# Kernel optimization log

Measured on AMD Instinct MI355X. Metric: run time of the kernel, lower is better.

Reference implementation:

```python
import jax, jax.numpy as jnp
import numpy as np

B, V, C, H, W, N = 2, 5, 32, 256, 320, 40000


def setup_inputs() -> dict:
    key = jax.random.key(0)
    k1, k2, k3, k4 = jax.random.split(key, 4)
    feature_maps = jax.random.normal(k1, (B, V, C, H, W), dtype=jnp.float32)
    # points with z in [1,4] and normalized image coords mostly inside the frustum
    z = jax.random.uniform(k2, (B, N), minval=1.0, maxval=4.0)
    xn = jax.random.uniform(k3, (B, N), minval=-0.55, maxval=0.55)
    yn = jax.random.uniform(k4, (B, N), minval=-0.45, maxval=0.45)
    pts = jnp.stack([xn * z, yn * z, z], axis=1)  # [B, 3, N]
    f = float(W)
    K = jnp.array([[f, 0.0, W / 2.0], [0.0, f, H / 2.0], [0.0, 0.0, 1.0]], jnp.float32)
    cam_intrinsics = jnp.broadcast_to(K, (B, V, 3, 3)).astype(jnp.float32)
    E = jnp.concatenate([jnp.eye(3, dtype=jnp.float32), jnp.zeros((3, 1), jnp.float32)], axis=1)
    cam_extrinsics = jnp.broadcast_to(E, (B, V, 3, 4)).astype(jnp.float32)
    return {"feature_maps": feature_maps, "pts": pts,
            "cam_intrinsics": cam_intrinsics, "cam_extrinsics": cam_extrinsics}


def _bilinear(fm_flat, gx, gy):
    """grid_sample, mode='bilinear', padding_mode='zeros', align_corners=False.
    fm_flat: [BV, C, H*W]; gx, gy: [BV, N] in [-1, 1]. Returns [BV, C, N]."""
    ix = ((gx + 1.0) * W - 1.0) * 0.5
    iy = ((gy + 1.0) * H - 1.0) * 0.5
    x0 = jnp.floor(ix)
    y0 = jnp.floor(iy)
    wx = ix - x0
    wy = iy - y0
    x0i = x0.astype(jnp.int32)
    y0i = y0.astype(jnp.int32)
    out = jnp.zeros((fm_flat.shape[0], fm_flat.shape[1], gx.shape[1]), fm_flat.dtype)
    corners = ((0, 0, (1.0 - wx) * (1.0 - wy)), (1, 0, wx * (1.0 - wy)),
               (0, 1, (1.0 - wx) * wy), (1, 1, wx * wy))
    for dx, dy, w in corners:
        xc = x0i + dx
        yc = y0i + dy
        valid = (xc >= 0) & (xc < W) & (yc >= 0) & (yc < H)
        idx = jnp.clip(yc, 0, H - 1) * W + jnp.clip(xc, 0, W - 1)  # [BV, N]
        v = jnp.take_along_axis(fm_flat, idx[:, None, :], axis=2)  # [BV, C, N]
        out = out + v * (w * valid)[:, None, :]
    return out


def _forward(feature_maps, pts, cam_intrinsics, cam_extrinsics):
    BV = B * V
    fm = feature_maps.reshape(BV, C, H, W)
    Km = cam_intrinsics.reshape(BV, 3, 3)
    Em = cam_extrinsics.reshape(BV, 3, 4)
    R = Em[:, :, :3]
    t = Em[:, :, 3:]
    pe = jnp.broadcast_to(pts[:, None], (B, V, 3, N)).reshape(BV, 3, N)
    tp = (R @ pe + t).transpose(0, 2, 1)  # [BV, N, 3] camera-space points
    x, y, z = tp[..., 0], tp[..., 1], tp[..., 2]
    nuv = jnp.stack([x / z, y / z, jnp.ones_like(x)], axis=-1)  # [BV, N, 3]
    uv = jnp.einsum('bnj,bij->bni', nuv, Km)[..., :2]  # pixel coords
    gx = (uv[..., 0] - 0.5) / (W - 1) * 2.0 - 1.0
    gy = (uv[..., 1] - 0.5) / (H - 1) * 2.0 - 1.0
    dx = 2.0 / (W - 1)
    dy = 2.0 / (H - 1)
    fm_flat = fm.reshape(BV, C, H * W)
    feat = _bilinear(fm_flat, gx, gy)
    fl = _bilinear(fm_flat, gx - dx, gy)
    fr = _bilinear(fm_flat, gx + dx, gy)
    ft = _bilinear(fm_flat, gx, gy - dy)
    fb = _bilinear(fm_flat, gx, gy + dy)
    grad_x = 0.5 * (fr - fl)
    grad_y = 0.5 * (fb - ft)
    pts_feature = feat.reshape(B, V, C, N)
    pts_feature_grad = jnp.stack([grad_x, grad_y], axis=-1).reshape(B, V, C, N, 2)
    return pts_feature, pts_feature_grad


def reference(feature_maps, pts, cam_intrinsics, cam_extrinsics):
    return _forward(feature_maps, pts, cam_intrinsics, cam_extrinsics)
```

## Files before the change

### kernel.cpp

```cpp
#include <hip/hip_runtime.h>

#define Bc 2
#define Vc 5
#define Cc 32
#define Hc 256
#define Wc 320
#define Nc 40000
#define HWc (Hc * Wc)

typedef float v2f __attribute__((ext_vector_type(2)));

__device__ __forceinline__ unsigned bf16_rn(float x) {
    unsigned u = __float_as_uint(x);
    return (u + 0x7fffu + ((u >> 16) & 1u)) >> 16;
}

__global__ void __launch_bounds__(256)
transpose_bf16_kernel(const float* __restrict__ fm, unsigned short* __restrict__ fmT)
{
    __shared__ float tile[Cc][65];
    const int bv  = blockIdx.y;
    const int hw0 = blockIdx.x * 64;
    const int t   = threadIdx.x;

    const int tx = t & 63;
    const int ty = t >> 6;
    const float* src = fm + (size_t)bv * Cc * HWc + hw0;
    #pragma unroll
    for (int i = 0; i < 8; ++i) {
        int c = ty * 8 + i;
        tile[c][tx] = __builtin_nontemporal_load(&src[(size_t)c * HWc + tx]);
    }
    __syncthreads();

    const int cq = t & 3;
    const int hw = t >> 2;
    unsigned r[4];
    #pragma unroll
    for (int j = 0; j < 4; ++j) {
        float a = tile[cq * 8 + 2 * j][hw];
        float b = tile[cq * 8 + 2 * j + 1][hw];
        r[j] = bf16_rn(a) | (bf16_rn(b) << 16);
    }
    const int half = cq >> 1;
    const int sub  = cq & 1;
    uint4* dst = (uint4*)fmT
               + ((size_t)(bv * 2 + half) * HWc + (hw0 + hw)) * 2 + sub;
    *dst = make_uint4(r[0], r[1], r[2], r[3]);
}

__device__ __forceinline__ void corner_setup(float ix, float iy, float coef,
                                             float wk[4], int pix[4])
{
    float x0f = floorf(ix), y0f = floorf(iy);
    float wx = ix - x0f, wy = iy - y0f;
    int x0 = (int)x0f, y0 = (int)y0f;
    float wg0 = (1.0f - wx) * (1.0f - wy);
    float wg1 = wx * (1.0f - wy);
    float wg2 = (1.0f - wx) * wy;
    float wg3 = wx * wy;
    float wg[4] = {wg0, wg1, wg2, wg3};
    #pragma unroll
    for (int k = 0; k < 4; ++k) {
        int xc = x0 + (k & 1);
        int yc = y0 + (k >> 1);
        bool valid = (xc >= 0) & (xc < Wc) & (yc >= 0) & (yc < Hc);
        wk[k] = valid ? coef * wg[k] : 0.0f;
        int xcl = min(max(xc, 0), Wc - 1);
        int ycl = min(max(yc, 0), Hc - 1);
        pix[k] = ycl * Wc + xcl;
    }
}

#define NBLK 6250
#define XQ   781
#define XR   2

__global__ void __launch_bounds__(256)
fgf_main(const unsigned short* __restrict__ fmT,
         const float* __restrict__ pts,
         const float* __restrict__ Kmat,
         const float* __restrict__ Emat,
         float* __restrict__ out_feat,
         float* __restrict__ out_grad)
{
    const int b0  = blockIdx.x;
    const int xcd = b0 & 7;
    const int i   = b0 >> 3;
    const int vb  = (xcd < XR) ? xcd * (XQ + 1) + i
                               : XR * (XQ + 1) + (xcd - XR) * XQ + i;

    const int v    = vb * 256 + (int)threadIdx.x;
    const int cq2  = v & 1;
    const int rest = v >> 1;
    const int n    = rest % Nc;
    const int bvh  = rest / Nc;
    const int bv   = bvh >> 1;
    const int half = bvh & 1;
    const int b    = bv / Vc;

    const float* p = pts + (size_t)(b * 3) * Nc + n;
    float px = p[0];
    float py = p[Nc];
    float pz = p[2 * Nc];

    const float* Ep = Emat + bv * 12;
    const float* Kp = Kmat + bv * 9;
    float x = Ep[0] * px + Ep[1] * py + Ep[2]  * pz + Ep[3];
    float y = Ep[4] * px + Ep[5] * py + Ep[6]  * pz + Ep[7];
    float z = Ep[8] * px + Ep[9] * py + Ep[10] * pz + Ep[11];
    float xz = x / z;
    float yz = y / z;
    float u = Kp[0] * xz + Kp[1] * yz + Kp[2];
    float vv = Kp[3] * xz + Kp[4] * yz + Kp[5];

    const float sxp = (float)Wc / (float)(Wc - 1);
    const float syp = (float)Hc / (float)(Hc - 1);
    float ix = (u  - 0.5f) * sxp - 0.5f;
    float iy = (vv - 0.5f) * syp - 0.5f;

    const uint4* base4 = (const uint4*)fmT + (size_t)bvh * (HWc * 2) + cq2;

    const float ox[5] = {0.0f, -sxp, sxp, 0.0f, 0.0f};
    const float oy[5] = {0.0f, 0.0f, 0.0f, -syp, syp};
    const float cf[5] = {1.0f, -0.5f, 0.5f, -0.5f, 0.5f};
    const int   as[5] = {0, 1, 1, 2, 2};

    float acc[3][8];
    #pragma unroll
    for (int a = 0; a < 3; ++a)
        #pragma unroll
        for (int j = 0; j < 8; ++j) acc[a][j] = 0.0f;

    float wk[2][4];
    int   pix[2][4];
    uint4 rg[2][4];

    corner_setup(ix + ox[0], iy + oy[0], cf[0], wk[0], pix[0]);
    #pragma unroll
    for (int k = 0; k < 4; ++k) rg[0][k] = base4[(unsigned)pix[0][k] * 2u];

    #pragma unroll
    for (int s = 0; s < 5; ++s) {
        int cur = s & 1;
        if (s < 4) {
            int nxt = cur ^ 1;
            corner_setup(ix + ox[s + 1], iy + oy[s + 1], cf[s + 1], wk[nxt], pix[nxt]);
            #pragma unroll
            for (int k = 0; k < 4; ++k) rg[nxt][k] = base4[(unsigned)pix[nxt][k] * 2u];
        }
        float* a = acc[as[s]];
        #pragma unroll
        for (int k = 0; k < 4; ++k) {
            uint4 w = rg[cur][k];
            float ww = wk[cur][k];
            a[0] = fmaf(ww, __uint_as_float(w.x << 16),          a[0]);
            a[1] = fmaf(ww, __uint_as_float(w.x & 0xffff0000u), a[1]);
            a[2] = fmaf(ww, __uint_as_float(w.y << 16),          a[2]);
            a[3] = fmaf(ww, __uint_as_float(w.y & 0xffff0000u), a[3]);
            a[4] = fmaf(ww, __uint_as_float(w.z << 16),          a[4]);
            a[5] = fmaf(ww, __uint_as_float(w.z & 0xffff0000u), a[5]);
            a[6] = fmaf(ww, __uint_as_float(w.w << 16),          a[6]);
            a[7] = fmaf(ww, __uint_as_float(w.w & 0xffff0000u), a[7]);
        }
    }

    const int cbase = half * 16 + cq2 * 8;
    size_t obase = (size_t)bv * Cc * Nc + n;
    v2f* gp = (v2f*)out_grad;
    #pragma unroll
    for (int j = 0; j < 8; ++j) {
        int c = cbase + j;
        __builtin_nontemporal_store(acc[0][j], &out_feat[obase + (size_t)c * Nc]);
        v2f g = {acc[1][j], acc[2][j]};
        __builtin_nontemporal_store(g, &gp[obase + (size_t)c * Nc]);
    }
}

__device__ __forceinline__ float fetch_px(const float* __restrict__ fm, int x, int y) {
    if (x < 0 || x >= Wc || y < 0 || y >= Hc) return 0.0f;
    return fm[y * Wc + x];
}
__device__ __forceinline__ float bilin(const float* __restrict__ fm, float ix, float iy) {
    float x0f = floorf(ix), y0f = floorf(iy);
    float wx = ix - x0f, wy = iy - y0f;
    int x0 = (int)x0f, y0 = (int)y0f;
    float v00 = fetch_px(fm, x0, y0);
    float v10 = fetch_px(fm, x0 + 1, y0);
    float v01 = fetch_px(fm, x0, y0 + 1);
    float v11 = fetch_px(fm, x0 + 1, y0 + 1);
    return (v00 * (1.0f - wx) + v10 * wx) * (1.0f - wy)
         + (v01 * (1.0f - wx) + v11 * wx) * wy;
}
__global__ void __launch_bounds__(256)
fgf_fallback(const float* __restrict__ fm,
             const float* __restrict__ pts,
             const float* __restrict__ Kmat,
             const float* __restrict__ Emat,
             float* __restrict__ out_feat,
             float* __restrict__ out_grad)
{
    int idx = blockIdx.x * 256 + threadIdx.x;
    const int total = Bc * Vc * Cc * Nc;
    if (idx >= total) return;
    int n = idx % Nc;
    int tcb = idx / Nc;
    int c = tcb % Cc;
    int bv = tcb / Cc;
    int b = bv / Vc;
    const float* p = pts + (size_t)(b * 3) * Nc + n;
    float px = p[0], py = p[Nc], pz = p[2 * Nc];
    const float* Ep = Emat + bv * 12;
    const float* Kp = Kmat + bv * 9;
    float x = Ep[0] * px + Ep[1] * py + Ep[2] * pz + Ep[3];
    float y = Ep[4] * px + Ep[5] * py + Ep[6] * pz + Ep[7];
    float z = Ep[8] * px + Ep[9] * py + Ep[10] * pz + Ep[11];
    float xz = x / z, yz = y / z;
    float u = Kp[0] * xz + Kp[1] * yz + Kp[2];
    float v = Kp[3] * xz + Kp[4] * yz + Kp[5];
    const float sxp = (float)Wc / (float)(Wc - 1);
    const float syp = (float)Hc / (float)(Hc - 1);
    float ix = (u - 0.5f) * sxp - 0.5f;
    float iy = (v - 0.5f) * syp - 0.5f;
    const float* f = fm + (size_t)(bv * Cc + c) * HWc;
    float feat = bilin(f, ix, iy);
    float fl = bilin(f, ix - sxp, iy);
    float fr = bilin(f, ix + sxp, iy);
    float ft = bilin(f, ix, iy - syp);
    float fb = bilin(f, ix, iy + syp);
    size_t o = (size_t)(bv * Cc + c) * Nc + n;
    out_feat[o] = feat;
    ((float2*)out_grad)[o] = make_float2(0.5f * (fr - fl), 0.5f * (fb - ft));
}

extern "C" void kernel_launch(void* const* d_in, const int* in_sizes, int n_in,
                              void* d_out, int out_size, void* d_ws, size_t ws_size,
                              hipStream_t stream) {
    const float* fm  = (const float*)d_in[0];
    const float* pts = (const float*)d_in[1];
    const float* K   = (const float*)d_in[2];
    const float* E   = (const float*)d_in[3];

    float* out_feat = (float*)d_out;
    float* out_grad = (float*)d_out + (size_t)Bc * Vc * Cc * Nc;

    const size_t fmT_bytes = (size_t)Bc * Vc * Cc * HWc * sizeof(unsigned short);

    if (ws_size >= fmT_bytes) {
        unsigned short* fmT = (unsigned short*)d_ws;
        dim3 tgrid(HWc / 64, Bc * Vc);
        transpose_bf16_kernel<<<tgrid, 256, 0, stream>>>(fm, fmT);
        fgf_main<<<NBLK, 256, 0, stream>>>(fmT, pts, K, E, out_feat, out_grad);
    } else {
        const int total = Bc * Vc * Cc * Nc;
        fgf_fallback<<<(total + 255) / 256, 256, 0, stream>>>(fm, pts, K, E, out_feat, out_grad);
    }
}
```

Measured before the change: 273.5 us.

## Share overlapping bilinear taps across the five samples in one stencil

The five separate 4-corner bilinear gathers (center, left, right, top, bottom) are replaced by one shared 12-pixel stencil around the center cell. Each pixel is loaded once and its contributions to the feature and both gradients are accumulated with precomputed weights. Rare cases where a shifted sample lands two cells away are handled by branches that load extra pixels. This cuts gathers per thread from 20 to 12. The XCD-aware block remapping is also dropped in favour of plain linear block indexing, which may change L2 locality across XCDs.

```diff
diff --git a/kernel.cpp b/kernel.cpp
--- a/kernel.cpp
+++ b/kernel.cpp
@@ -7,6 +7,8 @@
 #define Wc 320
 #define Nc 40000
 #define HWc (Hc * Wc)
+
+#define NMAIN ((Bc * Vc * 2 * Nc * 2) / 256)
 
 typedef float v2f __attribute__((ext_vector_type(2)));
 
@@ -49,32 +51,16 @@
     *dst = make_uint4(r[0], r[1], r[2], r[3]);
 }
 
-__device__ __forceinline__ void corner_setup(float ix, float iy, float coef,
-                                             float wk[4], int pix[4])
-{
-    float x0f = floorf(ix), y0f = floorf(iy);
-    float wx = ix - x0f, wy = iy - y0f;
-    int x0 = (int)x0f, y0 = (int)y0f;
-    float wg0 = (1.0f - wx) * (1.0f - wy);
-    float wg1 = wx * (1.0f - wy);
-    float wg2 = (1.0f - wx) * wy;
-    float wg3 = wx * wy;
-    float wg[4] = {wg0, wg1, wg2, wg3};
-    #pragma unroll
-    for (int k = 0; k < 4; ++k) {
-        int xc = x0 + (k & 1);
-        int yc = y0 + (k >> 1);
-        bool valid = (xc >= 0) & (xc < Wc) & (yc >= 0) & (yc < Hc);
-        wk[k] = valid ? coef * wg[k] : 0.0f;
-        int xcl = min(max(xc, 0), Wc - 1);
-        int ycl = min(max(yc, 0), Hc - 1);
-        pix[k] = ycl * Wc + xcl;
-    }
-}
-
-#define NBLK 6250
-#define XQ   781
-#define XR   2
+__device__ __forceinline__ void acc8(float* a, uint4 w, float s) {
+    a[0] = fmaf(s, __uint_as_float(w.x << 16),          a[0]);
+    a[1] = fmaf(s, __uint_as_float(w.x & 0xffff0000u), a[1]);
+    a[2] = fmaf(s, __uint_as_float(w.y << 16),          a[2]);
+    a[3] = fmaf(s, __uint_as_float(w.y & 0xffff0000u), a[3]);
+    a[4] = fmaf(s, __uint_as_float(w.z << 16),          a[4]);
+    a[5] = fmaf(s, __uint_as_float(w.z & 0xffff0000u), a[5]);
+    a[6] = fmaf(s, __uint_as_float(w.w << 16),          a[6]);
+    a[7] = fmaf(s, __uint_as_float(w.w & 0xffff0000u), a[7]);
+}
 
 __global__ void __launch_bounds__(256)
 fgf_main(const unsigned short* __restrict__ fmT,
@@ -84,13 +70,7 @@
          float* __restrict__ out_feat,
          float* __restrict__ out_grad)
 {
-    const int b0  = blockIdx.x;
-    const int xcd = b0 & 7;
-    const int i   = b0 >> 3;
-    const int vb  = (xcd < XR) ? xcd * (XQ + 1) + i
-                               : XR * (XQ + 1) + (xcd - XR) * XQ + i;
-
-    const int v    = vb * 256 + (int)threadIdx.x;
+    const int v    = blockIdx.x * 256 + (int)threadIdx.x;
     const int cq2  = v & 1;
     const int rest = v >> 1;
     const int n    = rest % Nc;
@@ -111,7 +91,7 @@
     float z = Ep[8] * px + Ep[9] * py + Ep[10] * pz + Ep[11];
     float xz = x / z;
     float yz = y / z;
-    float u = Kp[0] * xz + Kp[1] * yz + Kp[2];
+    float u  = Kp[0] * xz + Kp[1] * yz + Kp[2];
     float vv = Kp[3] * xz + Kp[4] * yz + Kp[5];
 
     const float sxp = (float)Wc / (float)(Wc - 1);
@@ -119,50 +99,147 @@
     float ix = (u  - 0.5f) * sxp - 0.5f;
     float iy = (vv - 0.5f) * syp - 0.5f;
 
+    float x0f = floorf(ix), y0f = floorf(iy);
+    float wx = ix - x0f, wy = iy - y0f;
+    int x0 = (int)x0f, y0 = (int)y0f;
+
+    float ixL = ix - sxp, ixR = ix + sxp;
+    float iyT = iy - syp, iyB = iy + syp;
+    float xLf = floorf(ixL), xRf = floorf(ixR);
+    float yTf = floorf(iyT), yBf = floorf(iyB);
+    float wLa = ixL - (x0f - 1.0f);
+    float wRa = ixR - (x0f + 1.0f);
+    float wTa = iyT - (y0f - 1.0f);
+    float wBa = iyB - (y0f + 1.0f);
+    bool mL = xLf < x0f - 1.5f;
+    bool mR = xRf > x0f + 1.5f;
+    bool mT = yTf < y0f - 1.5f;
+    bool mB = yBf > y0f + 1.5f;
+
+    float cx0 = 1.0f - wx, cx1 = wx;
+    float cy0 = 1.0f - wy, cy1 = wy;
+    float gw0 = -0.5f * (1.0f - wLa);
+    float gw1 = -0.5f * wLa;
+    float gw2 =  0.5f * (1.0f - wRa);
+    float gw3 =  0.5f * wRa;
+    float gym  = -0.5f * (1.0f - wTa);
+    float gyr0 = -0.5f * wTa;
+    float gyr1 =  0.5f * (1.0f - wBa);
+    float gyp  =  0.5f * wBa;
+
+    float vxm1 = ((unsigned)(x0 - 1) < (unsigned)Wc) ? 1.0f : 0.0f;
+    float vx00 = ((unsigned)(x0    ) < (unsigned)Wc) ? 1.0f : 0.0f;
+    float vx01 = ((unsigned)(x0 + 1) < (unsigned)Wc) ? 1.0f : 0.0f;
+    float vx02 = ((unsigned)(x0 + 2) < (unsigned)Wc) ? 1.0f : 0.0f;
+    float vym1 = ((unsigned)(y0 - 1) < (unsigned)Hc) ? 1.0f : 0.0f;
+    float vy00 = ((unsigned)(y0    ) < (unsigned)Hc) ? 1.0f : 0.0f;
+    float vy01 = ((unsigned)(y0 + 1) < (unsigned)Hc) ? 1.0f : 0.0f;
+    float vy02 = ((unsigned)(y0 + 2) < (unsigned)Hc) ? 1.0f : 0.0f;
+
     const uint4* base4 = (const uint4*)fmT + (size_t)bvh * (HWc * 2) + cq2;
-
-    const float ox[5] = {0.0f, -sxp, sxp, 0.0f, 0.0f};
-    const float oy[5] = {0.0f, 0.0f, 0.0f, -syp, syp};
-    const float cf[5] = {1.0f, -0.5f, 0.5f, -0.5f, 0.5f};
-    const int   as[5] = {0, 1, 1, 2, 2};
+    int cxm1 = min(max(x0 - 1, 0), Wc - 1);
+    int cx0b = min(max(x0,     0), Wc - 1);
+    int cx1b = min(max(x0 + 1, 0), Wc - 1);
+    int cx2b = min(max(x0 + 2, 0), Wc - 1);
+    int ry0  = min(max(y0,     0), Hc - 1) * Wc;
+    int ry1  = min(max(y0 + 1, 0), Hc - 1) * Wc;
+    int rym1 = min(max(y0 - 1, 0), Hc - 1) * Wc;
+    int ry2  = min(max(y0 + 2, 0), Hc - 1) * Wc;
+
+    uint4 P00 = base4[(unsigned)(ry0 + cxm1) * 2u];
+    uint4 P01 = base4[(unsigned)(ry0 + cx0b) * 2u];
+    uint4 P02 = base4[(unsigned)(ry0 + cx1b) * 2u];
+    uint4 P03 = base4[(unsigned)(ry0 + cx2b) * 2u];
+    uint4 P10 = base4[(unsigned)(ry1 + cxm1) * 2u];
+    uint4 P11 = base4[(unsigned)(ry1 + cx0b) * 2u];
+    uint4 P12 = base4[(unsigned)(ry1 + cx1b) * 2u];
+    uint4 P13 = base4[(unsigned)(ry1 + cx2b) * 2u];
+    uint4 Qt0 = base4[(unsigned)(rym1 + cx0b) * 2u];
+    uint4 Qt1 = base4[(unsigned)(rym1 + cx1b) * 2u];
+    uint4 Qb0 = base4[(unsigned)(ry2 + cx0b) * 2u];
+    uint4 Qb1 = base4[(unsigned)(ry2 + cx1b) * 2u];
 
     float acc[3][8];
     #pragma unroll
     for (int a = 0; a < 3; ++a)
         #pragma unroll
         for (int j = 0; j < 8; ++j) acc[a][j] = 0.0f;
-
-    float wk[2][4];
-    int   pix[2][4];
-    uint4 rg[2][4];
-
-    corner_setup(ix + ox[0], iy + oy[0], cf[0], wk[0], pix[0]);
-    #pragma unroll
-    for (int k = 0; k < 4; ++k) rg[0][k] = base4[(unsigned)pix[0][k] * 2u];
-
-    #pragma unroll
-    for (int s = 0; s < 5; ++s) {
-        int cur = s & 1;
-        if (s < 4) {
-            int nxt = cur ^ 1;
-            corner_setup(ix + ox[s + 1], iy + oy[s + 1], cf[s + 1], wk[nxt], pix[nxt]);
-            #pragma unroll
-            for (int k = 0; k < 4; ++k) rg[nxt][k] = base4[(unsigned)pix[nxt][k] * 2u];
-        }
-        float* a = acc[as[s]];
-        #pragma unroll
-        for (int k = 0; k < 4; ++k) {
-            uint4 w = rg[cur][k];
-            float ww = wk[cur][k];
-            a[0] = fmaf(ww, __uint_as_float(w.x << 16),          a[0]);
-            a[1] = fmaf(ww, __uint_as_float(w.x & 0xffff0000u), a[1]);
-            a[2] = fmaf(ww, __uint_as_float(w.y << 16),          a[2]);
-            a[3] = fmaf(ww, __uint_as_float(w.y & 0xffff0000u), a[3]);
-            a[4] = fmaf(ww, __uint_as_float(w.z << 16),          a[4]);
-            a[5] = fmaf(ww, __uint_as_float(w.z & 0xffff0000u), a[5]);
-            a[6] = fmaf(ww, __uint_as_float(w.w << 16),          a[6]);
-            a[7] = fmaf(ww, __uint_as_float(w.w & 0xffff0000u), a[7]);
-        }
+    float* f  = acc[0];
+    float* gx = acc[1];
+    float* gy = acc[2];
+
+    acc8(f,  P01, cx0 * cy0 * vx00 * vy00);
+    acc8(f,  P02, cx1 * cy0 * vx01 * vy00);
+    acc8(gx, P00, gw0 * cy0 * vxm1 * vy00);
+    acc8(gx, P01, gw1 * cy0 * vx00 * vy00);
+    acc8(gx, P02, gw2 * cy0 * vx01 * vy00);
+    acc8(gx, P03, gw3 * cy0 * vx02 * vy00);
+    acc8(gy, P01, gyr0 * cx0 * vx00 * vy00);
+    acc8(gy, P02, gyr0 * cx1 * vx01 * vy00);
+    acc8(f,  P11, cx0 * cy1 * vx00 * vy01);
+    acc8(f,  P12, cx1 * cy1 * vx01 * vy01);
+    acc8(gx, P10, gw0 * cy1 * vxm1 * vy01);
+    acc8(gx, P11, gw1 * cy1 * vx00 * vy01);
+    acc8(gx, P12, gw2 * cy1 * vx01 * vy01);
+    acc8(gx, P13, gw3 * cy1 * vx02 * vy01);
+    acc8(gy, P11, gyr1 * cx0 * vx00 * vy01);
+    acc8(gy, P12, gyr1 * cx1 * vx01 * vy01);
+    acc8(gy, Qt0, gym * cx0 * vx00 * vym1);
+    acc8(gy, Qt1, gym * cx1 * vx01 * vym1);
+    acc8(gy, Qb0, gyp * cx0 * vx00 * vy02);
+    acc8(gy, Qb1, gyp * cx1 * vx01 * vy02);
+
+    if (mL) {
+        int cxm2 = min(max(x0 - 2, 0), Wc - 1);
+        uint4 M0 = base4[(unsigned)(ry0 + cxm2) * 2u];
+        uint4 M1 = base4[(unsigned)(ry1 + cxm2) * 2u];
+        float vxm2 = ((unsigned)(x0 - 2) < (unsigned)Wc) ? 1.0f : 0.0f;
+        float s = 0.5f * wLa;
+        acc8(gx, M0,   s * cy0 * vxm2 * vy00);
+        acc8(gx, P00, -2.0f * s * cy0 * vxm1 * vy00);
+        acc8(gx, P01,  s * cy0 * vx00 * vy00);
+        acc8(gx, M1,   s * cy1 * vxm2 * vy01);
+        acc8(gx, P10, -2.0f * s * cy1 * vxm1 * vy01);
+        acc8(gx, P11,  s * cy1 * vx00 * vy01);
+    }
+    if (mR) {
+        int cx3 = min(max(x0 + 3, 0), Wc - 1);
+        uint4 M0 = base4[(unsigned)(ry0 + cx3) * 2u];
+        uint4 M1 = base4[(unsigned)(ry1 + cx3) * 2u];
+        float vx03 = ((unsigned)(x0 + 3) < (unsigned)Wc) ? 1.0f : 0.0f;
+        float e = 0.5f * (wRa - 1.0f);
+        acc8(gx, P02,  e * cy0 * vx01 * vy00);
+        acc8(gx, P03, -2.0f * e * cy0 * vx02 * vy00);
+        acc8(gx, M0,   e * cy0 * vx03 * vy00);
+        acc8(gx, P12,  e * cy1 * vx01 * vy01);
+        acc8(gx, P13, -2.0f * e * cy1 * vx02 * vy01);
+        acc8(gx, M1,   e * cy1 * vx03 * vy01);
+    }
+    if (mT) {
+        int rym2 = min(max(y0 - 2, 0), Hc - 1) * Wc;
+        uint4 M0 = base4[(unsigned)(rym2 + cx0b) * 2u];
+        uint4 M1 = base4[(unsigned)(rym2 + cx1b) * 2u];
+        float vym2 = ((unsigned)(y0 - 2) < (unsigned)Hc) ? 1.0f : 0.0f;
+        float s = 0.5f * wTa;
+        acc8(gy, M0,   s * cx0 * vx00 * vym2);
+        acc8(gy, Qt0, -2.0f * s * cx0 * vx00 * vym1);
+        acc8(gy, P01,  s * cx0 * vx00 * vy00);
+        acc8(gy, M1,   s * cx1 * vx01 * vym2);
+        acc8(gy, Qt1, -2.0f * s * cx1 * vx01 * vym1);
+        acc8(gy, P02,  s * cx1 * vx01 * vy00);
+    }
+    if (mB) {
+        int ry3 = min(max(y0 + 3, 0), Hc - 1) * Wc;
+        uint4 M0 = base4[(unsigned)(ry3 + cx0b) * 2u];
+        uint4 M1 = base4[(unsigned)(ry3 + cx1b) * 2u];
+        float vy03 = ((unsigned)(y0 + 3) < (unsigned)Hc) ? 1.0f : 0.0f;
+        float e = 0.5f * (wBa - 1.0f);
+        acc8(gy, P11,  e * cx0 * vx00 * vy01);
+        acc8(gy, Qb0, -2.0f * e * cx0 * vx00 * vy02);
+        acc8(gy, M0,   e * cx0 * vx00 * vy03);
+        acc8(gy, P12,  e * cx1 * vx01 * vy01);
+        acc8(gy, Qb1, -2.0f * e * cx1 * vx01 * vy02);
+        acc8(gy, M1,   e * cx1 * vx01 * vy03);
     }
 
     const int cbase = half * 16 + cq2 * 8;
@@ -250,7 +327,7 @@
         unsigned short* fmT = (unsigned short*)d_ws;
         dim3 tgrid(HWc / 64, Bc * Vc);
         transpose_bf16_kernel<<<tgrid, 256, 0, stream>>>(fm, fmT);
-        fgf_main<<<NBLK, 256, 0, stream>>>(fmT, pts, K, E, out_feat, out_grad);
+        fgf_main<<<NMAIN, 256, 0, stream>>>(fmT, pts, K, E, out_feat, out_grad);
     } else {
         const int total = Bc * Vc * Cc * Nc;
         fgf_fallback<<<(total + 255) / 256, 256, 0, stream>>>(fm, pts, K, E, out_feat, out_grad);
```

New measurement: 275.7 us. Within noise of the previous version (+0.8%).
